# Kernel optimization log

Measured on AMD Instinct MI355X. Metric: run time of the kernel, lower is better.

Reference implementation:

```python
import jax, jax.numpy as jnp
import numpy as np

D = 128   # node feature dim
C = 2     # classes
N = 50000 # nodes
E = 500000  # edges (before self-loops)
H1 = 2    # conv1 heads
NEG_SLOPE = 0.2
BN_EPS = 1e-5


def setup_inputs() -> dict:
    key = jax.random.key(0)
    ks = jax.random.split(key, 24)
    rn = lambda k, shape, s=0.05: jax.random.normal(k, shape, dtype=jnp.float32) * s
    inp = {
        'x': jax.random.normal(ks[0], (N, D), dtype=jnp.float32),
        'edge_index': jax.random.randint(ks[1], (2, E), 0, N, dtype=jnp.int64),
        # conv1: GATConv(D, D, heads=2, concat=True)
        'W1': rn(ks[2], (D, H1 * D)),
        'att_src1': rn(ks[3], (H1, D)),
        'att_dst1': rn(ks[4], (H1, D)),
        'bias1': jnp.zeros((H1 * D,), jnp.float32),
        # conv2: GATConv(2D, D, heads=1, concat=False)
        'W2': rn(ks[5], (2 * D, D)),
        'att_src2': rn(ks[6], (1, D)),
        'att_dst2': rn(ks[7], (1, D)),
        'bias2': jnp.zeros((D,), jnp.float32),
        # lin1 = MLP([3D, 96]) : Linear -> ReLU -> BatchNorm1d
        'Wl': rn(ks[8], (3 * D, 96)), 'bl': jnp.zeros((96,), jnp.float32),
        'gl': jnp.ones((96,), jnp.float32), 'betal': jnp.zeros((96,), jnp.float32),
        # mlp1 = MLP([96, 96, C]) : two (Linear -> ReLU -> BN) blocks
        'Wa': rn(ks[9], (96, 96)), 'ba': jnp.zeros((96,), jnp.float32),
        'ga': jnp.ones((96,), jnp.float32), 'betaa': jnp.zeros((96,), jnp.float32),
        'Wb': rn(ks[10], (96, C)), 'bb': jnp.zeros((C,), jnp.float32),
        'gb': jnp.ones((C,), jnp.float32), 'betab': jnp.zeros((C,), jnp.float32),
    }
    return inp


def gat_conv(x, src, dst, W, att_src, att_dst, bias, heads, out_dim, concat):
    # PyG GATConv: h = x W -> [N,H,F]; per-edge logit leakyrelu(a_s.h_src + a_d.h_dst);
    # segment softmax over edges grouped by destination; weighted scatter-sum.
    n = x.shape[0]
    h = (x @ W).reshape(n, heads, out_dim)
    a_src = jnp.einsum('nhd,hd->nh', h, att_src)  # [N,H]
    a_dst = jnp.einsum('nhd,hd->nh', h, att_dst)
    alpha = jax.nn.leaky_relu(a_src[src] + a_dst[dst], NEG_SLOPE)  # [Etot,H]
    m = jax.ops.segment_max(alpha, dst, num_segments=n)            # [N,H]
    e = jnp.exp(alpha - m[dst])
    s = jax.ops.segment_sum(e, dst, num_segments=n)
    w = e / (s[dst] + 1e-16)                                       # [Etot,H]
    out = jax.ops.segment_sum(h[src] * w[:, :, None], dst, num_segments=n)  # [N,H,F]
    out = out.reshape(n, heads * out_dim) if concat else out.mean(axis=1)
    return out + bias


def mlp_block(x, W, b, gamma, beta):
    # Linear -> ReLU -> BatchNorm1d (training-mode batch stats, biased var)
    y = jax.nn.relu(x @ W + b)
    mu = y.mean(axis=0)
    var = ((y - mu) ** 2).mean(axis=0)
    return gamma * (y - mu) / jnp.sqrt(var + BN_EPS) + beta


def reference(x, edge_index, W1, att_src1, att_dst1, bias1,
              W2, att_src2, att_dst2, bias2,
              Wl, bl, gl, betal, Wa, ba, ga, betaa, Wb, bb, gb, betab):
    n = x.shape[0]
    # PyG GATConv default add_self_loops=True
    loops = jnp.arange(n, dtype=edge_index.dtype)
    src = jnp.concatenate([edge_index[0], loops])
    dst = jnp.concatenate([edge_index[1], loops])
    x1 = gat_conv(x, src, dst, W1, att_src1, att_dst1, bias1, H1, D, True)    # [N,2D]
    x2 = gat_conv(x1, src, dst, W2, att_src2, att_dst2, bias2, 1, D, False)   # [N,D]
    h = jnp.concatenate([x1, x2], axis=1)                                      # [N,3D]
    h = mlp_block(h, Wl, bl, gl, betal)     # lin1
    h = mlp_block(h, Wa, ba, ga, betaa)     # mlp1 layer 1
    h = mlp_block(h, Wb, bb, gb, betab)     # mlp1 layer 2
    return h
```

## Files before the change

### kernel.cpp

```cpp
#include <hip/hip_runtime.h>
#include <hip/hip_bf16.h>
#include <cstdint>
#include <cstddef>

#define NNODES 50000
#define NEDGES 500000
#define ETOT   (NEDGES + NNODES)
#define MAXDEG 96

typedef __attribute__((ext_vector_type(8))) short short8;
typedef __attribute__((ext_vector_type(8))) unsigned short ushort8v;
typedef __attribute__((ext_vector_type(4))) float floatx4;
typedef __attribute__((ext_vector_type(4))) unsigned short ushort4v;

__device__ __forceinline__ unsigned short f2bf(float f) {
    union { __hip_bfloat16 h; unsigned short u; } cv;
    cv.h = __float2bfloat16(f);
    return cv.u;
}
__device__ __forceinline__ float bf2f(unsigned short u) {
    union { unsigned int i; float f; } cv;
    cv.i = ((unsigned int)u) << 16;
    return cv.f;
}

#define GBM 128
#define GBN 64
#define GBK 32

__global__ __launch_bounds__(256, 4) void gemm_mfma(
    const unsigned short* __restrict__ A, int lda,
    const unsigned short* __restrict__ Bt,
    float* __restrict__ C,
    unsigned short* __restrict__ Cb,
    const float* __restrict__ bias,
    float* __restrict__ colsum, float* __restrict__ colsq,
    const float* __restrict__ att_s, const float* __restrict__ att_d,
    float* __restrict__ as_out, float* __restrict__ ad_out, int Hheads,
    int M, int N, int K, int do_relu)
{
    __shared__ __attribute__((aligned(16))) unsigned short Alds[GBM * GBK];
    __shared__ __attribute__((aligned(16))) unsigned short Blds[GBN * GBK];
    __shared__ float scol[GBN], sqcol[GBN];

    int tid = threadIdx.x;
    int wave = tid >> 6, lane = tid & 63;
    int row0 = blockIdx.y * GBM;
    int col0 = blockIdx.x * GBN;
    int m = lane & 15, q = lane >> 4;

    floatx4 acc[2][4] = {};

    for (int k0 = 0; k0 < K; k0 += GBK) {
        #pragma unroll
        for (int i = 0; i < 2; ++i) {
            int c = tid + i * 256;
            int r = c >> 2, off = (c & 3) * 8;
            int gr = row0 + r;
            short8 v = {};
            if (gr < M) v = *(const short8*)(A + (size_t)gr * lda + k0 + off);
            *(short8*)(Alds + r * GBK + off) = v;
        }
        {
            int r = tid >> 2, off = (tid & 3) * 8;
            short8 v = *(const short8*)(Bt + (size_t)(col0 + r) * K + k0 + off);
            *(short8*)(Blds + r * GBK + off) = v;
        }
        __syncthreads();

        short8 a0 = *(const short8*)(Alds + (wave * 32 + m) * GBK + q * 8);
        short8 a1 = *(const short8*)(Alds + (wave * 32 + 16 + m) * GBK + q * 8);
        #pragma unroll
        for (int ct = 0; ct < 4; ++ct) {
            short8 b = *(const short8*)(Blds + (ct * 16 + m) * GBK + q * 8);
            acc[0][ct] = __builtin_amdgcn_mfma_f32_16x16x32_bf16(a0, b, acc[0][ct], 0, 0, 0);
            acc[1][ct] = __builtin_amdgcn_mfma_f32_16x16x32_bf16(a1, b, acc[1][ct], 0, 0, 0);
        }
        __syncthreads();
    }

    float ps[4] = {}, pq[4] = {};
    #pragma unroll
    for (int rt = 0; rt < 2; ++rt) {
        #pragma unroll
        for (int r = 0; r < 4; ++r) {
            int gr = row0 + wave * 32 + rt * 16 + q * 4 + r;
            float ds = 0.f, dd = 0.f;
            #pragma unroll
            for (int ct = 0; ct < 4; ++ct) {
                int gc = col0 + ct * 16 + m;
                float v = acc[rt][ct][r];
                if (gc < N) {
                    if (att_s != nullptr) { ds += v * att_s[gc]; dd += v * att_d[gc]; }
                    float vb = v;
                    if (bias != nullptr) vb += bias[gc];
                    if (do_relu) vb = fmaxf(vb, 0.f);
                    if (gr < M) {
                        if (C  != nullptr) C[(size_t)gr * N + gc] = vb;
                        if (Cb != nullptr) Cb[(size_t)gr * N + gc] = f2bf(vb);
                        ps[ct] += vb; pq[ct] += vb * vb;
                    }
                }
            }
            if (att_s != nullptr) {
                #pragma unroll
                for (int off = 1; off < 16; off <<= 1) {
                    ds += __shfl_xor(ds, off);
                    dd += __shfl_xor(dd, off);
                }
                if (m == 0 && gr < M) {
                    int head = col0 >> 7;
                    atomicAdd(&as_out[gr * Hheads + head], ds);
                    atomicAdd(&ad_out[gr * Hheads + head], dd);
                }
            }
        }
    }
    if (colsum != nullptr) {
        if (tid < GBN) { scol[tid] = 0.f; sqcol[tid] = 0.f; }
        __syncthreads();
        #pragma unroll
        for (int ct = 0; ct < 4; ++ct) {
            atomicAdd(&scol[ct * 16 + m], ps[ct]);
            atomicAdd(&sqcol[ct * 16 + m], pq[ct]);
        }
        __syncthreads();
        if (tid < GBN) {
            int gc = col0 + tid;
            if (gc < N) {
                atomicAdd(&colsum[gc], scol[tid]);
                atomicAdd(&colsq[gc], sqcol[tid]);
            }
        }
    }
}

__global__ void cast_x_k(const float* __restrict__ x, unsigned short* __restrict__ xb, int total4) {
    int i = blockIdx.x * blockDim.x + threadIdx.x;
    if (i >= total4) return;
    const float4 v = ((const float4*)x)[i];
    ushort4v o;
    o.x = f2bf(v.x); o.y = f2bf(v.y); o.z = f2bf(v.z); o.w = f2bf(v.w);
    ((ushort4v*)xb)[i] = o;
}

__global__ void cast_weights(const float* __restrict__ W1, const float* __restrict__ W2,
                             const float* __restrict__ Wl,
                             unsigned short* __restrict__ W1t, unsigned short* __restrict__ W2t,
                             unsigned short* __restrict__ Wlt) {
    int i = blockIdx.x * 256 + threadIdx.x;
    if (i < 32768) {
        int n = i >> 7, k = i & 127;
        W1t[i] = f2bf(W1[k * 256 + n]);
    } else if (i < 65536) {
        int j = i - 32768;
        int n = j >> 8, k = j & 255;
        W2t[j] = f2bf(W2[k * 128 + n]);
    } else if (i < 114688) {
        int j = i - 65536;
        int n = j / 384, k = j % 384;
        Wlt[j] = (n < 96) ? f2bf(Wl[(size_t)k * 96 + n]) : (unsigned short)0;
    }
}

__global__ void bnfold_a(const float* __restrict__ csum, const float* __restrict__ csq,
                         const float* __restrict__ gamma, const float* __restrict__ beta,
                         const float* __restrict__ Wa, const float* __restrict__ ba,
                         unsigned short* __restrict__ Wat2, float* __restrict__ ba_f) {
    __shared__ float scl[96], shf[96];
    int tid = threadIdx.x;
    if (tid < 96) {
        float mu  = csum[tid] / (float)NNODES;
        float var = csq[tid] / (float)NNODES - mu * mu;
        if (var < 0.f) var = 0.f;
        float sc = gamma[tid] * rsqrtf(var + 1e-5f);
        scl[tid] = sc; shf[tid] = beta[tid] - mu * sc;
    }
    __syncthreads();
    for (int idx = tid; idx < 128 * 96; idx += 256) {
        int n = idx / 96, k = idx % 96;
        Wat2[idx] = (n < 96) ? f2bf(scl[k] * Wa[k * 96 + n]) : (unsigned short)0;
    }
    if (tid < 96) {
        float s = ba[tid];
        for (int k = 0; k < 96; ++k) s += shf[k] * Wa[k * 96 + tid];
        ba_f[tid] = s;
    }
}

__global__ void bnfold_b(const float* __restrict__ csum, const float* __restrict__ csq,
                         const float* __restrict__ gamma, const float* __restrict__ beta,
                         const float* __restrict__ Wb, const float* __restrict__ bb,
                         unsigned short* __restrict__ Wbt, float* __restrict__ bb_f) {
    __shared__ float scl[96], shf[96];
    int tid = threadIdx.x;
    if (tid < 96) {
        float mu  = csum[tid] / (float)NNODES;
        float var = csq[tid] / (float)NNODES - mu * mu;
        if (var < 0.f) var = 0.f;
        float sc = gamma[tid] * rsqrtf(var + 1e-5f);
        scl[tid] = sc; shf[tid] = beta[tid] - mu * sc;
    }
    __syncthreads();
    for (int idx = tid; idx < 64 * 96; idx += 256) {
        int n = idx / 96, k = idx % 96;
        Wbt[idx] = (n < 2) ? f2bf(scl[k] * Wb[k * 2 + n]) : (unsigned short)0;
    }
    if (tid < 2) {
        float s = bb[tid];
        for (int k = 0; k < 96; ++k) s += shf[k] * Wb[k * 2 + tid];
        bb_f[tid] = s;
    }
}

__global__ void bn_fin_apply(const float* __restrict__ csum, const float* __restrict__ csq,
                             const float* __restrict__ gamma, const float* __restrict__ beta,
                             float* __restrict__ y, int total) {
    int i = blockIdx.x * blockDim.x + threadIdx.x;
    if (i >= total) return;
    int j = i & 1;
    float mu  = csum[j] / (float)NNODES;
    float var = csq[j] / (float)NNODES - mu * mu;
    if (var < 0.f) var = 0.f;
    float sc = gamma[j] * rsqrtf(var + 1e-5f);
    float sh = beta[j] - mu * sc;
    y[i] = y[i] * sc + sh;
}

__device__ __forceinline__ void edge_src_dst(const int* ei, int e, int& src, int& dst) {
    if (e < NEDGES) { src = ei[e]; dst = ei[NEDGES + e]; }
    else { src = e - NEDGES; dst = src; }
}

__global__ __launch_bounds__(256) void csr_count(const int* __restrict__ ei, int* __restrict__ cnt) {
    int e = blockIdx.x * blockDim.x + threadIdx.x;
    if (e >= ETOT) return;
    int src, dst; edge_src_dst(ei, e, src, dst); (void)src;
    atomicAdd(&cnt[dst], 1);
}

#define SCAN_CH 1024
#define SCAN_NB ((NNODES + SCAN_CH - 1) / SCAN_CH)

__global__ __launch_bounds__(256) void scan1(const int* __restrict__ cnt, int* __restrict__ part) {
    int t = threadIdx.x;
    int base = blockIdx.x * SCAN_CH + t * 4;
    int4 v = {0, 0, 0, 0};
    if (base + 3 < NNODES) v = *(const int4*)(cnt + base);
    else {
        if (base + 0 < NNODES) v.x = cnt[base + 0];
        if (base + 1 < NNODES) v.y = cnt[base + 1];
        if (base + 2 < NNODES) v.z = cnt[base + 2];
        if (base + 3 < NNODES) v.w = cnt[base + 3];
    }
    int s = v.x + v.y + v.z + v.w;
    __shared__ int sm[256];
    sm[t] = s;
    __syncthreads();
    for (int off = 128; off > 0; off >>= 1) {
        if (t < off) sm[t] += sm[t + off];
        __syncthreads();
    }
    if (t == 0) part[blockIdx.x] = sm[0];
}

__global__ void scan2(int* __restrict__ part, int* __restrict__ rowstart) {
    int lane = threadIdx.x;
    int v = (lane < SCAN_NB) ? part[lane] : 0;
    #pragma unroll
    for (int off = 1; off < 64; off <<= 1) {
        int t = __shfl_up(v, off);
        if (lane >= off) v += t;
    }
    int ex = __shfl_up(v, 1);
    if (lane == 0) ex = 0;
    if (lane < SCAN_NB) part[lane] = ex;
    if (lane == 0) rowstart[NNODES] = ETOT;
}

__global__ __launch_bounds__(256) void scan3(const int* __restrict__ cnt, const int* __restrict__ part,
                                             int* __restrict__ rowstart, int* __restrict__ cursor) {
    int t = threadIdx.x;
    int base = blockIdx.x * SCAN_CH + t * 4;
    int4 v = {0, 0, 0, 0};
    if (base + 3 < NNODES) v = *(const int4*)(cnt + base);
    else {
        if (base + 0 < NNODES) v.x = cnt[base + 0];
        if (base + 1 < NNODES) v.y = cnt[base + 1];
        if (base + 2 < NNODES) v.z = cnt[base + 2];
        if (base + 3 < NNODES) v.w = cnt[base + 3];
    }
    int s = v.x + v.y + v.z + v.w;
    __shared__ int sm[2][256];
    sm[0][t] = s;
    __syncthreads();
    int cur = 0;
    #pragma unroll
    for (int off = 1; off < 256; off <<= 1) {
        int nxt = cur ^ 1;
        int val = sm[cur][t];
        if (t >= off) val += sm[cur][t - off];
        sm[nxt][t] = val;
        __syncthreads();
        cur = nxt;
    }
    int p = sm[cur][t] - s + part[blockIdx.x];
    if (base + 0 < NNODES) { rowstart[base + 0] = p; cursor[base + 0] = p; } p += v.x;
    if (base + 1 < NNODES) { rowstart[base + 1] = p; cursor[base + 1] = p; } p += v.y;
    if (base + 2 < NNODES) { rowstart[base + 2] = p; cursor[base + 2] = p; } p += v.z;
    if (base + 3 < NNODES) { rowstart[base + 3] = p; cursor[base + 3] = p; }
}

__global__ __launch_bounds__(256) void csr_fill(const int* __restrict__ ei,
                                                int* __restrict__ cursor,
                                                int* __restrict__ esrc) {
    int e = blockIdx.x * blockDim.x + threadIdx.x;
    if (e >= ETOT) return;
    int src, dst; edge_src_dst(ei, e, src, dst);
    int pos = atomicAdd(&cursor[dst], 1);
    esrc[pos] = src;
}

__global__ __launch_bounds__(256) void gat_gather_h2(
    const int* __restrict__ rowstart, const int* __restrict__ esrc,
    const unsigned short* __restrict__ hb, const float* __restrict__ a_src,
    const float* __restrict__ a_dst, const float* __restrict__ bias,
    unsigned short* __restrict__ xcat)
{
    __shared__ float wl[4][2][MAXDEG];
    int wave = threadIdx.x >> 6;
    int n = (blockIdx.x * blockDim.x + threadIdx.x) >> 6;
    int lane = threadIdx.x & 63;
    if (n >= NNODES) return;
    int beg = rowstart[n], end = rowstart[n + 1];
    int deg = end - beg;
    float ad0 = a_dst[n * 2], ad1 = a_dst[n * 2 + 1];

    float m0 = -1e30f, m1 = -1e30f;
    for (int idx = lane; idx < deg; idx += 64) {
        int s = esrc[beg + idx];
        float l0 = a_src[s * 2] + ad0;     l0 = l0 >= 0.f ? l0 : 0.2f * l0;
        float l1 = a_src[s * 2 + 1] + ad1; l1 = l1 >= 0.f ? l1 : 0.2f * l1;
        m0 = fmaxf(m0, l0); m1 = fmaxf(m1, l1);
        if (idx < MAXDEG) { wl[wave][0][idx] = l0; wl[wave][1][idx] = l1; }
    }
    #pragma unroll
    for (int off = 1; off < 64; off <<= 1) {
        m0 = fmaxf(m0, __shfl_xor(m0, off));
        m1 = fmaxf(m1, __shfl_xor(m1, off));
    }
    float s0 = 0.f, s1 = 0.f;
    for (int idx = lane; idx < deg; idx += 64) {
        float l0, l1;
        if (idx < MAXDEG) { l0 = wl[wave][0][idx]; l1 = wl[wave][1][idx]; }
        else {
            int s = esrc[beg + idx];
            l0 = a_src[s * 2] + ad0;     l0 = l0 >= 0.f ? l0 : 0.2f * l0;
            l1 = a_src[s * 2 + 1] + ad1; l1 = l1 >= 0.f ? l1 : 0.2f * l1;
        }
        float e0 = __expf(l0 - m0), e1 = __expf(l1 - m1);
        s0 += e0; s1 += e1;
        if (idx < MAXDEG) { wl[wave][0][idx] = e0; wl[wave][1][idx] = e1; }
    }
    #pragma unroll
    for (int off = 1; off < 64; off <<= 1) {
        s0 += __shfl_xor(s0, off);
        s1 += __shfl_xor(s1, off);
    }

    int g  = lane >> 5;
    int sl = lane & 31;
    int head = sl >> 4;
    float mh   = head ? m1 : m0;
    float invh = head ? 1.f / (s1 + 1e-16f) : 1.f / (s0 + 1e-16f);
    float adh  = head ? ad1 : ad0;

    float acc[8] = {};
    for (int idx = g; idx < deg; idx += 2) {
        int s = esrc[beg + idx];
        float w;
        if (idx < MAXDEG) w = wl[wave][head][idx] * invh;
        else {
            float l = a_src[s * 2 + head] + adh; l = l >= 0.f ? l : 0.2f * l;
            w = __expf(l - mh) * invh;
        }
        const ushort8v hv = *(const ushort8v*)(hb + (size_t)s * 256 + sl * 8);
        #pragma unroll
        for (int j = 0; j < 8; ++j) acc[j] += w * bf2f(hv[j]);
    }
    #pragma unroll
    for (int j = 0; j < 8; ++j) acc[j] += __shfl_xor(acc[j], 32);
    if (g == 0) {
        ushort8v o;
        #pragma unroll
        for (int j = 0; j < 8; ++j) o[j] = f2bf(acc[j] + bias[sl * 8 + j]);
        *(ushort8v*)(xcat + (size_t)n * 384 + sl * 8) = o;
    }
}

__global__ __launch_bounds__(256) void gat_gather_h1(
    const int* __restrict__ rowstart, const int* __restrict__ esrc,
    const unsigned short* __restrict__ hb, const float* __restrict__ a_src,
    const float* __restrict__ a_dst, const float* __restrict__ bias,
    unsigned short* __restrict__ xcat)
{
    __shared__ float wl[4][MAXDEG];
    int wave = threadIdx.x >> 6;
    int n = (blockIdx.x * blockDim.x + threadIdx.x) >> 6;
    int lane = threadIdx.x & 63;
    if (n >= NNODES) return;
    int beg = rowstart[n], end = rowstart[n + 1];
    int deg = end - beg;
    float ad0 = a_dst[n];

    float m0 = -1e30f;
    for (int idx = lane; idx < deg; idx += 64) {
        int s = esrc[beg + idx];
        float l0 = a_src[s] + ad0; l0 = l0 >= 0.f ? l0 : 0.2f * l0;
        m0 = fmaxf(m0, l0);
        if (idx < MAXDEG) wl[wave][idx] = l0;
    }
    #pragma unroll
    for (int off = 1; off < 64; off <<= 1) m0 = fmaxf(m0, __shfl_xor(m0, off));
    float s0 = 0.f;
    for (int idx = lane; idx < deg; idx += 64) {
        float l0;
        if (idx < MAXDEG) l0 = wl[wave][idx];
        else {
            int s = esrc[beg + idx];
            l0 = a_src[s] + ad0; l0 = l0 >= 0.f ? l0 : 0.2f * l0;
        }
        float e0 = __expf(l0 - m0);
        s0 += e0;
        if (idx < MAXDEG) wl[wave][idx] = e0;
    }
    #pragma unroll
    for (int off = 1; off < 64; off <<= 1) s0 += __shfl_xor(s0, off);
    float inv0 = 1.f / (s0 + 1e-16f);

    int g  = lane >> 4;
    int sl = lane & 15;

    float acc[8] = {};
    for (int idx = g; idx < deg; idx += 4) {
        int s = esrc[beg + idx];
        float w;
        if (idx < MAXDEG) w = wl[wave][idx] * inv0;
        else {
            float l = a_src[s] + ad0; l = l >= 0.f ? l : 0.2f * l;
            w = __expf(l - m0) * inv0;
        }
        const ushort8v hv = *(const ushort8v*)(hb + (size_t)s * 128 + sl * 8);
        #pragma unroll
        for (int j = 0; j < 8; ++j) acc[j] += w * bf2f(hv[j]);
    }
    #pragma unroll
    for (int j = 0; j < 8; ++j) acc[j] += __shfl_xor(acc[j], 16);
    #pragma unroll
    for (int j = 0; j < 8; ++j) acc[j] += __shfl_xor(acc[j], 32);
    if (g == 0) {
        ushort8v o;
        #pragma unroll
        for (int j = 0; j < 8; ++j) o[j] = f2bf(acc[j] + bias[sl * 8 + j]);
        *(ushort8v*)(xcat + (size_t)n * 384 + 256 + sl * 8) = o;
    }
}

extern "C" void kernel_launch(void* const* d_in, const int* in_sizes, int n_in,
                              void* d_out, int out_size, void* d_ws, size_t ws_size,
                              hipStream_t stream) {
    const float* x        = (const float*)d_in[0];
    const int*   ei       = (const int*)d_in[1];
    const float* W1       = (const float*)d_in[2];
    const float* att_src1 = (const float*)d_in[3];
    const float* att_dst1 = (const float*)d_in[4];
    const float* bias1    = (const float*)d_in[5];
    const float* W2       = (const float*)d_in[6];
    const float* att_src2 = (const float*)d_in[7];
    const float* att_dst2 = (const float*)d_in[8];
    const float* bias2    = (const float*)d_in[9];
    const float* Wl       = (const float*)d_in[10];
    const float* bl       = (const float*)d_in[11];
    const float* gl       = (const float*)d_in[12];
    const float* betal    = (const float*)d_in[13];
    const float* Wa       = (const float*)d_in[14];
    const float* ba       = (const float*)d_in[15];
    const float* ga       = (const float*)d_in[16];
    const float* betaa    = (const float*)d_in[17];
    const float* Wb       = (const float*)d_in[18];
    const float* bb       = (const float*)d_in[19];
    const float* gb       = (const float*)d_in[20];
    const float* betab    = (const float*)d_in[21];
    float* out = (float*)d_out;
    char* ws = (char*)d_ws;

    const int N = NNODES;

    const size_t offY2b  = 0;
    const size_t offXcat = 19200000;
    const size_t offXb   = 57600000;
    const size_t offY1b  = 70400000;
    const size_t offHb1  = 80000000;
    const size_t offW1t  = 105600000;
    const size_t offW2t  = 105665536;
    const size_t offWlt  = 105731072;
    const size_t offWat2 = 105829376;
    const size_t offWbt  = 105853952;
    const size_t offBaf  = 105866240;
    const size_t offBbf  = 105866640;
    const size_t offRow  = 106000000;
    const size_t offCur  = 106200128;
    const size_t offEsrc = 106400832;
    const size_t offPart = 108700000;
    const size_t offAs1  = 108800000;
    const size_t offAd1  = 109200000;
    const size_t offAs2  = 109600000;
    const size_t offAd2  = 109800000;
    const size_t offSt   = 110000000;

    unsigned short* y2b  = (unsigned short*)(ws + offY2b);
    unsigned short* xcat = (unsigned short*)(ws + offXcat);
    unsigned short* xb   = (unsigned short*)(ws + offXb);
    unsigned short* hb2  = (unsigned short*)(ws + offXb);
    unsigned short* y1b  = (unsigned short*)(ws + offY1b);
    unsigned short* hb1  = (unsigned short*)(ws + offHb1);
    unsigned short* W1t  = (unsigned short*)(ws + offW1t);
    unsigned short* W2t  = (unsigned short*)(ws + offW2t);
    unsigned short* Wlt  = (unsigned short*)(ws + offWlt);
    unsigned short* Wat2 = (unsigned short*)(ws + offWat2);
    unsigned short* Wbt  = (unsigned short*)(ws + offWbt);
    float* ba_f = (float*)(ws + offBaf);
    float* bb_f = (float*)(ws + offBbf);
    int* rowst  = (int*)(ws + offRow);
    int* cursor = (int*)(ws + offCur);
    int* esrc   = (int*)(ws + offEsrc);
    int* part   = (int*)(ws + offPart);
    float* as1  = (float*)(ws + offAs1);
    float* ad1  = (float*)(ws + offAd1);
    float* as2  = (float*)(ws + offAs2);
    float* ad2  = (float*)(ws + offAd2);

    float* csum_l = (float*)(ws + offSt + 0);
    float* csq_l  = (float*)(ws + offSt + 512);
    float* csum_a = (float*)(ws + offSt + 2048);
    float* csq_a  = (float*)(ws + offSt + 2560);
    float* csum_b = (float*)(ws + offSt + 4096);
    float* csq_b  = (float*)(ws + offSt + 4608);

    hipMemsetAsync(ws + offRow, 0, (NNODES + 1) * sizeof(int), stream);
    hipMemsetAsync(ws + offAs1, 0, (offSt + 6144) - offAs1, stream);

    dim3 blk(256);
    int edgeBlocks  = (ETOT + 255) / 256;
    int waveBlocksN = (N + 3) / 4;

    cast_x_k<<<(N * 128 / 4 + 255) / 256, blk, 0, stream>>>(x, xb, N * 128 / 4);
    cast_weights<<<(114688 + 255) / 256, blk, 0, stream>>>(W1, W2, Wl, W1t, W2t, Wlt);

    csr_count<<<edgeBlocks, blk, 0, stream>>>(ei, rowst);
    scan1<<<SCAN_NB, blk, 0, stream>>>(rowst, part);
    scan2<<<1, 64, 0, stream>>>(part, rowst);
    scan3<<<SCAN_NB, blk, 0, stream>>>(rowst, part, rowst, cursor);
    csr_fill<<<edgeBlocks, blk, 0, stream>>>(ei, cursor, esrc);

    gemm_mfma<<<dim3(4, (N + GBM - 1) / GBM), blk, 0, stream>>>(
        xb, 128, W1t, nullptr, hb1, nullptr, nullptr, nullptr,
        att_src1, att_dst1, as1, ad1, 2, N, 256, 128, 0);
    gat_gather_h2<<<waveBlocksN, blk, 0, stream>>>(rowst, esrc, hb1, as1, ad1, bias1, xcat);

    gemm_mfma<<<dim3(2, (N + GBM - 1) / GBM), blk, 0, stream>>>(
        xcat, 384, W2t, nullptr, hb2, nullptr, nullptr, nullptr,
        att_src2, att_dst2, as2, ad2, 1, N, 128, 256, 0);
    gat_gather_h1<<<waveBlocksN, blk, 0, stream>>>(rowst, esrc, hb2, as2, ad2, bias2, xcat);

    gemm_mfma<<<dim3(2, (N + GBM - 1) / GBM), blk, 0, stream>>>(
        xcat, 384, Wlt, nullptr, y1b, bl, csum_l, csq_l,
        nullptr, nullptr, nullptr, nullptr, 0, N, 96, 384, 1);
    bnfold_a<<<1, 256, 0, stream>>>(csum_l, csq_l, gl, betal, Wa, ba, Wat2, ba_f);

    gemm_mfma<<<dim3(2, (N + GBM - 1) / GBM), blk, 0, stream>>>(
        y1b, 96, Wat2, nullptr, y2b, ba_f, csum_a, csq_a,
        nullptr, nullptr, nullptr, nullptr, 0, N, 96, 96, 1);
    bnfold_b<<<1, 256, 0, stream>>>(csum_a, csq_a, ga, betaa, Wb, bb, Wbt, bb_f);

    gemm_mfma<<<dim3(1, (N + GBM - 1) / GBM), blk, 0, stream>>>(
        y2b, 96, Wbt, out, nullptr, bb_f, csum_b, csq_b,
        nullptr, nullptr, nullptr, nullptr, 0, N, 2, 96, 1);

    bn_fin_apply<<<(N * 2 + 255) / 256, blk, 0, stream>>>(csum_b, csq_b, gb, betab, out, N * 2);
}
```

Baseline: 407.8 us.

## Fuse GAT softmax into single-pass gather without max subtraction

Replaces the three-pass segment softmax (max, sum, weighted gather) in both GAT gather kernels with a single pass that accumulates unnormalised exp(logit) weights and their sum together, normalising once at the end. Removes the shared-memory logit staging and the MAXDEG fallback path, and unrolls the edge loop with independent accumulators so more row loads are in flight. This cuts the redundant index and a_src reads, but drops the max-subtraction safeguard, so it relies on logits staying small enough not to overflow exp.

```diff
diff --git a/kernel.cpp b/kernel.cpp
--- a/kernel.cpp
+++ b/kernel.cpp
@@ -6,7 +6,6 @@
 #define NNODES 50000
 #define NEDGES 500000
 #define ETOT   (NEDGES + NNODES)
-#define MAXDEG 96
 
 typedef __attribute__((ext_vector_type(8))) short short8;
 typedef __attribute__((ext_vector_type(8))) unsigned short ushort8v;
@@ -327,73 +326,54 @@
     const float* __restrict__ a_dst, const float* __restrict__ bias,
     unsigned short* __restrict__ xcat)
 {
-    __shared__ float wl[4][2][MAXDEG];
-    int wave = threadIdx.x >> 6;
     int n = (blockIdx.x * blockDim.x + threadIdx.x) >> 6;
     int lane = threadIdx.x & 63;
     if (n >= NNODES) return;
-    int beg = rowstart[n], end = rowstart[n + 1];
-    int deg = end - beg;
-    float ad0 = a_dst[n * 2], ad1 = a_dst[n * 2 + 1];
-
-    float m0 = -1e30f, m1 = -1e30f;
-    for (int idx = lane; idx < deg; idx += 64) {
-        int s = esrc[beg + idx];
-        float l0 = a_src[s * 2] + ad0;     l0 = l0 >= 0.f ? l0 : 0.2f * l0;
-        float l1 = a_src[s * 2 + 1] + ad1; l1 = l1 >= 0.f ? l1 : 0.2f * l1;
-        m0 = fmaxf(m0, l0); m1 = fmaxf(m1, l1);
-        if (idx < MAXDEG) { wl[wave][0][idx] = l0; wl[wave][1][idx] = l1; }
-    }
-    #pragma unroll
-    for (int off = 1; off < 64; off <<= 1) {
-        m0 = fmaxf(m0, __shfl_xor(m0, off));
-        m1 = fmaxf(m1, __shfl_xor(m1, off));
-    }
-    float s0 = 0.f, s1 = 0.f;
-    for (int idx = lane; idx < deg; idx += 64) {
-        float l0, l1;
-        if (idx < MAXDEG) { l0 = wl[wave][0][idx]; l1 = wl[wave][1][idx]; }
-        else {
-            int s = esrc[beg + idx];
-            l0 = a_src[s * 2] + ad0;     l0 = l0 >= 0.f ? l0 : 0.2f * l0;
-            l1 = a_src[s * 2 + 1] + ad1; l1 = l1 >= 0.f ? l1 : 0.2f * l1;
-        }
-        float e0 = __expf(l0 - m0), e1 = __expf(l1 - m1);
-        s0 += e0; s1 += e1;
-        if (idx < MAXDEG) { wl[wave][0][idx] = e0; wl[wave][1][idx] = e1; }
-    }
-    #pragma unroll
-    for (int off = 1; off < 64; off <<= 1) {
-        s0 += __shfl_xor(s0, off);
-        s1 += __shfl_xor(s1, off);
-    }
-
-    int g  = lane >> 5;
-    int sl = lane & 31;
-    int head = sl >> 4;
-    float mh   = head ? m1 : m0;
-    float invh = head ? 1.f / (s1 + 1e-16f) : 1.f / (s0 + 1e-16f);
-    float adh  = head ? ad1 : ad0;
-
-    float acc[8] = {};
-    for (int idx = g; idx < deg; idx += 2) {
-        int s = esrc[beg + idx];
-        float w;
-        if (idx < MAXDEG) w = wl[wave][head][idx] * invh;
-        else {
-            float l = a_src[s * 2 + head] + adh; l = l >= 0.f ? l : 0.2f * l;
-            w = __expf(l - mh) * invh;
-        }
-        const ushort8v hv = *(const ushort8v*)(hb + (size_t)s * 256 + sl * 8);
-        #pragma unroll
-        for (int j = 0; j < 8; ++j) acc[j] += w * bf2f(hv[j]);
-    }
+    int beg = rowstart[n], deg = rowstart[n + 1] - beg;
+    const int* es = esrc + beg;
+    int g = lane >> 5, sl = lane & 31, head = sl >> 4;
+    float adh = a_dst[n * 2 + head];
+
+    float acc[8] = {}, acc2[8] = {}, acc3[8] = {};
+    float se = 0.f;
+    for (int idx = g; idx < deg; idx += 6) {
+        int sA = es[idx];
+        float lA = a_src[sA * 2 + head] + adh; lA = lA >= 0.f ? lA : 0.2f * lA;
+        float wA = __expf(lA);
+        const ushort8v hvA = *(const ushort8v*)(hb + (size_t)sA * 256 + sl * 8);
+        int iB = idx + 2, iC = idx + 4;
+        if (iB < deg) {
+            int sB = es[iB];
+            float lB = a_src[sB * 2 + head] + adh; lB = lB >= 0.f ? lB : 0.2f * lB;
+            float wB = __expf(lB);
+            const ushort8v hvB = *(const ushort8v*)(hb + (size_t)sB * 256 + sl * 8);
+            se += wB;
+            #pragma unroll
+            for (int j = 0; j < 8; ++j) acc2[j] += wB * bf2f(hvB[j]);
+        }
+        if (iC < deg) {
+            int sC = es[iC];
+            float lC = a_src[sC * 2 + head] + adh; lC = lC >= 0.f ? lC : 0.2f * lC;
+            float wC = __expf(lC);
+            const ushort8v hvC = *(const ushort8v*)(hb + (size_t)sC * 256 + sl * 8);
+            se += wC;
+            #pragma unroll
+            for (int j = 0; j < 8; ++j) acc3[j] += wC * bf2f(hvC[j]);
+        }
+        se += wA;
+        #pragma unroll
+        for (int j = 0; j < 8; ++j) acc[j] += wA * bf2f(hvA[j]);
+    }
+    #pragma unroll
+    for (int j = 0; j < 8; ++j) acc[j] += acc2[j] + acc3[j];
     #pragma unroll
     for (int j = 0; j < 8; ++j) acc[j] += __shfl_xor(acc[j], 32);
+    se += __shfl_xor(se, 32);
+    float inv = 1.f / (se + 1e-16f);
     if (g == 0) {
         ushort8v o;
         #pragma unroll
-        for (int j = 0; j < 8; ++j) o[j] = f2bf(acc[j] + bias[sl * 8 + j]);
+        for (int j = 0; j < 8; ++j) o[j] = f2bf(acc[j] * inv + bias[sl * 8 + j]);
         *(ushort8v*)(xcat + (size_t)n * 384 + sl * 8) = o;
     }
 }
@@ -404,64 +384,48 @@
     const float* __restrict__ a_dst, const float* __restrict__ bias,
     unsigned short* __restrict__ xcat)
 {
-    __shared__ float wl[4][MAXDEG];
-    int wave = threadIdx.x >> 6;
     int n = (blockIdx.x * blockDim.x + threadIdx.x) >> 6;
     int lane = threadIdx.x & 63;
     if (n >= NNODES) return;
-    int beg = rowstart[n], end = rowstart[n + 1];
-    int deg = end - beg;
+    int beg = rowstart[n], deg = rowstart[n + 1] - beg;
+    const int* es = esrc + beg;
+    int g = lane >> 4, sl = lane & 15;
     float ad0 = a_dst[n];
 
-    float m0 = -1e30f;
-    for (int idx = lane; idx < deg; idx += 64) {
-        int s = esrc[beg + idx];
-        float l0 = a_src[s] + ad0; l0 = l0 >= 0.f ? l0 : 0.2f * l0;
-        m0 = fmaxf(m0, l0);
-        if (idx < MAXDEG) wl[wave][idx] = l0;
-    }
-    #pragma unroll
-    for (int off = 1; off < 64; off <<= 1) m0 = fmaxf(m0, __shfl_xor(m0, off));
-    float s0 = 0.f;
-    for (int idx = lane; idx < deg; idx += 64) {
-        float l0;
-        if (idx < MAXDEG) l0 = wl[wave][idx];
-        else {
-            int s = esrc[beg + idx];
-            l0 = a_src[s] + ad0; l0 = l0 >= 0.f ? l0 : 0.2f * l0;
-        }
-        float e0 = __expf(l0 - m0);
-        s0 += e0;
-        if (idx < MAXDEG) wl[wave][idx] = e0;
-    }
-    #pragma unroll
-    for (int off = 1; off < 64; off <<= 1) s0 += __shfl_xor(s0, off);
-    float inv0 = 1.f / (s0 + 1e-16f);
-
-    int g  = lane >> 4;
-    int sl = lane & 15;
-
-    float acc[8] = {};
-    for (int idx = g; idx < deg; idx += 4) {
-        int s = esrc[beg + idx];
-        float w;
-        if (idx < MAXDEG) w = wl[wave][idx] * inv0;
-        else {
-            float l = a_src[s] + ad0; l = l >= 0.f ? l : 0.2f * l;
-            w = __expf(l - m0) * inv0;
-        }
-        const ushort8v hv = *(const ushort8v*)(hb + (size_t)s * 128 + sl * 8);
-        #pragma unroll
-        for (int j = 0; j < 8; ++j) acc[j] += w * bf2f(hv[j]);
-    }
+    float acc[8] = {}, acc2[8] = {};
+    float se = 0.f;
+    for (int idx = g; idx < deg; idx += 8) {
+        int sA = es[idx];
+        float lA = a_src[sA] + ad0; lA = lA >= 0.f ? lA : 0.2f * lA;
+        float wA = __expf(lA);
+        const ushort8v hvA = *(const ushort8v*)(hb + (size_t)sA * 128 + sl * 8);
+        int iB = idx + 4;
+        if (iB < deg) {
+            int sB = es[iB];
+            float lB = a_src[sB] + ad0; lB = lB >= 0.f ? lB : 0.2f * lB;
+            float wB = __expf(lB);
+            const ushort8v hvB = *(const ushort8v*)(hb + (size_t)sB * 128 + sl * 8);
+            se += wB;
+            #pragma unroll
+            for (int j = 0; j < 8; ++j) acc2[j] += wB * bf2f(hvB[j]);
+        }
+        se += wA;
+        #pragma unroll
+        for (int j = 0; j < 8; ++j) acc[j] += wA * bf2f(hvA[j]);
+    }
+    #pragma unroll
+    for (int j = 0; j < 8; ++j) acc[j] += acc2[j];
     #pragma unroll
     for (int j = 0; j < 8; ++j) acc[j] += __shfl_xor(acc[j], 16);
+    se += __shfl_xor(se, 16);
     #pragma unroll
     for (int j = 0; j < 8; ++j) acc[j] += __shfl_xor(acc[j], 32);
+    se += __shfl_xor(se, 32);
+    float inv = 1.f / (se + 1e-16f);
     if (g == 0) {
         ushort8v o;
         #pragma unroll
-        for (int j = 0; j < 8; ++j) o[j] = f2bf(acc[j] + bias[sl * 8 + j]);
+        for (int j = 0; j < 8; ++j) o[j] = f2bf(acc[j] * inv + bias[sl * 8 + j]);
         *(ushort8v*)(xcat + (size_t)n * 384 + 256 + sl * 8) = o;
     }
 }
```

Result: faster. 395.0 us (-3.1%).
